# Optimization experiments

Measured on AMD Instinct MI355X. Metric: run time of the kernel, lower is better.

The kernel has to match this reference:

```python
import jax, jax.numpy as jnp
import numpy as np

H = W = 64      # patch grid (shape)
WS = 8          # window_size
SHIFT = 4       # shift_size (SW-MSA)
HEAD_DIM = 32
N = WS * WS     # tokens per window


def _rel_position_index(ws):
    coords = np.stack(np.meshgrid(np.arange(ws), np.arange(ws), indexing='ij'))  # (2, ws, ws)
    cf = coords.reshape(2, -1)
    rel = cf[:, :, None] - cf[:, None, :]            # (2, N, N)
    rel = rel.transpose(1, 2, 0).astype(np.int64)    # (N, N, 2)
    rel[..., 0] += ws - 1
    rel[..., 1] += ws - 1
    rel[..., 0] *= 2 * ws - 1
    return (rel[..., 0] + rel[..., 1]).astype(np.int32)  # (N, N), values in [0,(2ws-1)^2)


def _shift_mask(h, w, ws, shift):
    # Swin cyclic-shift attention mask: (num_windows, N, N) with 0 / -100
    img = np.zeros((h, w), dtype=np.float32)
    cnt = 0
    slices = (slice(0, -ws), slice(-ws, -shift), slice(-shift, None))
    for hs in slices:
        for ws_ in slices:
            img[hs, ws_] = cnt
            cnt += 1
    win = img.reshape(h // ws, ws, w // ws, ws).transpose(0, 2, 1, 3).reshape(-1, ws * ws)
    diff = win[:, None, :] - win[:, :, None]
    return np.where(diff != 0, np.float32(-100.0), np.float32(0.0))


def setup_inputs() -> dict:
    key = jax.random.key(0)
    ks = jax.random.split(key, 6)
    dim = 384
    B = 32
    sd = 1.0 / np.sqrt(dim)
    return {
        'x': jax.random.normal(ks[0], (B, H * W, dim), jnp.float32),
        'qkv_w': jax.random.normal(ks[1], (dim, 3 * dim), jnp.float32) * sd,
        'qkv_b': jnp.zeros((3 * dim,), jnp.float32),
        'proj_w': jax.random.normal(ks[2], (dim, dim), jnp.float32) * sd,
        'proj_b': jnp.zeros((dim,), jnp.float32),
        'bias_table': jax.random.normal(ks[3], ((2 * WS - 1) ** 2, dim // HEAD_DIM), jnp.float32) * 0.02,
        'rel_index': jnp.asarray(_rel_position_index(WS)),
    }


def reference(x, qkv_w, qkv_b, proj_w, proj_b, bias_table, rel_index):
    B, L, C = x.shape
    heads = C // HEAD_DIM
    scale = HEAD_DIM ** -0.5
    nh, nw = H // WS, W // WS

    xg = x.reshape(B, H, W, C)
    if SHIFT > 0:
        xg = jnp.roll(xg, shift=(-SHIFT, -SHIFT), axis=(1, 2))

    # window partition -> (B*nWin, N, C)
    xw = xg.reshape(B, nh, WS, nw, WS, C).transpose(0, 1, 3, 2, 4, 5).reshape(B * nh * nw, N, C)

    qkv = xw @ qkv_w + qkv_b                              # (Bw, N, 3C)
    q, k, v = jnp.split(qkv, 3, axis=-1)
    def heads_first(t):
        return t.reshape(-1, N, heads, HEAD_DIM).transpose(0, 2, 1, 3)  # (Bw, h, N, d)
    q, k, v = heads_first(q), heads_first(k), heads_first(v)

    attn = jnp.einsum('bhnd,bhmd->bhnm', q * scale, k)    # (Bw, h, N, N)
    bias = bias_table[rel_index]                          # (N, N, h)
    attn = attn + bias.transpose(2, 0, 1)[None]

    if SHIFT > 0:
        mask = jnp.asarray(_shift_mask(H, W, WS, SHIFT))  # (nWin, N, N), trace-time constant
        attn = attn.reshape(B, nh * nw, heads, N, N) + mask[None, :, None]
        attn = attn.reshape(B * nh * nw, heads, N, N)

    attn = jax.nn.softmax(attn, axis=-1)
    out = jnp.einsum('bhnm,bhmd->bhnd', attn, v)          # (Bw, h, N, d)
    out = out.transpose(0, 2, 1, 3).reshape(B * nh * nw, N, C)
    out = out @ proj_w + proj_b

    # window reverse
    out = out.reshape(B, nh, nw, WS, WS, C).transpose(0, 1, 3, 2, 4, 5).reshape(B, H, W, C)
    if SHIFT > 0:
        out = jnp.roll(out, shift=(SHIFT, SHIFT), axis=(1, 2))
    return out.reshape(B, L, C)
```

## Files before the change

### kernel.cpp

```cpp
#include <hip/hip_runtime.h>
#include <hip/hip_bf16.h>

#define CDIM 384
#define NQKV 1152
#define HEADS 12
#define SHIFT_ 4
#define SCALE_Q 0.17677669529663687f

typedef __attribute__((ext_vector_type(8))) short bf16x8;
typedef __attribute__((ext_vector_type(4))) float f32x4;
typedef __attribute__((ext_vector_type(4))) float float4_t;
typedef __attribute__((ext_vector_type(4))) unsigned u32x4;
typedef __attribute__((ext_vector_type(2))) unsigned u32x2;

__device__ inline short f2bf(float f) {
    union { float f; unsigned u; } v; v.f = f;
    unsigned r = v.u + 0x7FFFu + ((v.u >> 16) & 1u);
    return (short)(r >> 16);
}

__device__ inline unsigned cvtpk(float lo, float hi) {
    unsigned r;
    asm("v_cvt_pk_bf16_f32 %0, %1, %2" : "=v"(r) : "v"(lo), "v"(hi));
    return r;
}

__device__ inline bf16x8 mk8(unsigned w0, unsigned w1, unsigned w2, unsigned w3) {
    u32x4 t = {w0, w1, w2, w3};
    return __builtin_bit_cast(bf16x8, t);
}

__device__ inline bf16x8 pack8(float4_t a, float4_t b) {
    return mk8(cvtpk(a[0], a[1]), cvtpk(a[2], a[3]),
               cvtpk(b[0], b[1]), cvtpk(b[2], b[3]));
}

__device__ inline bf16x8 regroup(unsigned p0, unsigned p1, unsigned p2,
                                 unsigned p3, int lane) {
    int lhi = (lane >> 4) & 3;
    int s0 = (lane & 15) + ((lhi & 1) ? 32 : 0);
    int s1 = s0 + 16;
    unsigned a0 = __shfl(p0, s0), b0 = __shfl(p2, s0);
    unsigned a1 = __shfl(p1, s0), b1 = __shfl(p3, s0);
    unsigned a2 = __shfl(p0, s1), b2 = __shfl(p2, s1);
    unsigned a3 = __shfl(p1, s1), b3 = __shfl(p3, s1);
    bool hi = lhi >= 2;
    return mk8(hi ? b0 : a0, hi ? b1 : a1, hi ? b2 : a2, hi ? b3 : a3);
}

__device__ inline void gl16(const short* g, const short* l) {
    __builtin_amdgcn_global_load_lds((const __attribute__((address_space(1))) void*)g,
                                     (__attribute__((address_space(3))) void*)l, 16, 0, 0);
}

__device__ inline int invswz(int c) {
    int b2 = (c >> 2) & 1, b3 = (c >> 3) & 1, b4 = (c >> 4) & 1;
    return (c & ~7) | ((b2 ^ b4) << 2) | (((((c >> 1) & 1)) ^ b3) << 1) | ((c & 1) ^ b2 ^ b4);
}

__device__ inline int region_id(int wIdx, int tok) {
    int gh = ((wIdx >> 3) << 3) + (tok >> 3);
    int gw = (wIdx & 7) * 8 + (tok & 7);
    int rh = gh < 56 ? 0 : (gh < 60 ? 1 : 2);
    int rw = gw < 56 ? 0 : (gw < 60 ? 1 : 2);
    return rh * 3 + rw;
}

__device__ inline int crow(int row) { return row * 136 + (row >> 3) * 8; }

__device__ inline size_t xrow(int mg) {
    int tok = mg & 63, win = mg >> 6;
    int b = win >> 6, wIdx = win & 63;
    int gh = ((wIdx >> 3) << 3) + (tok >> 3);
    int gw = (wIdx & 7) * 8 + (tok & 7);
    int sh_ = (gh + SHIFT_) & 63, sw_ = (gw + SHIFT_) & 63;
    return (size_t)(b * 4096 + sh_ * 64 + sw_) * CDIM;
}

__global__ void prep_kernel(const float* __restrict__ qkv_w,
                            const float* __restrict__ proj_w,
                            const float* __restrict__ bias_table,
                            const int* __restrict__ rel_index,
                            short* __restrict__ qkvwt,
                            short* __restrict__ projwt,
                            float* __restrict__ biasP) {
    int t = blockIdx.x * 256 + threadIdx.x;
    if (t < NQKV * CDIM) {
        int n = t / CDIM, k = t - n * CDIM;
        qkvwt[t] = f2bf(qkv_w[k * NQKV + n]);
    }
    if (t < CDIM * CDIM) {
        int n = t / CDIM, k = t - n * CDIM;
        projwt[t] = f2bf(proj_w[k * CDIM + n]);
    }
    if (t < HEADS * 16 * 64 * 4) {
        int r = t & 3, lane = (t >> 2) & 63, g = (t >> 8) & 15, h = t >> 12;
        int kt = g >> 2, qt = g & 3;
        int key = kt * 16 + (lane >> 4) * 4 + r;
        int query = qt * 16 + (lane & 15);
        biasP[t] = bias_table[rel_index[query * 64 + key] * HEADS + h];
    }
}

__global__ __launch_bounds__(256) void gemm_qkv(
    const float* __restrict__ x, const short* __restrict__ wt,
    const float* __restrict__ qkv_b, short* __restrict__ qkbuf,
    short* __restrict__ vT)
{
    __shared__ alignas(16) char smemb[35072];
    short* As = (short*)smemb;
    short* Bs = As + 8192;
    short* Cst = (short*)smemb;
    int tid = threadIdx.x;
    int hw = blockIdx.x;
    int lb = (hw & 7) * 1152 + (hw >> 3);
    int bm = lb / 9, bn = lb - bm * 9;
    int m0 = bm * 128, n0 = bn * 128;

    int lane = tid & 63, wv = tid >> 6;
    int c0 = wv * 128 + lane, c1 = c0 + 64;
    const float* Asrc0 = x + xrow(m0 + (c0 >> 2)) + (c0 & 3) * 8;
    const float* Asrc1 = x + xrow(m0 + (c1 >> 2)) + (c1 & 3) * 8;
    short* Aw0 = As + (c0 ^ ((c0 >> 2) & 7)) * 8;
    short* Aw1 = As + (c1 ^ ((c1 >> 2) & 7)) * 8;
    int l0 = invswz(c0), l1 = invswz(c1);
    const short* Bg0 = wt + (size_t)(n0 + (l0 >> 2)) * CDIM + (l0 & 3) * 8;
    const short* Bg1 = wt + (size_t)(n0 + (l1 >> 2)) * CDIM + (l1 & 3) * 8;
    short* Bdst0 = Bs + wv * 1024;
    short* Bdst1 = Bdst0 + 512;

    int wr = wv >> 1, wc = wv & 1;
    int lrow = lane & 15, lhi = lane >> 4;
    int arow = wr * 64 + lrow, brow = wc * 64 + lrow;
    const short* ard = As + ((((arow * 64 + lhi * 16)) ^ ((lrow & 7) << 4)) >> 1);
    const short* brd = Bs + ((((brow * 64 + lhi * 16)) ^ ((lrow & 7) << 4)) >> 1);

    f32x4 zero = {0.f, 0.f, 0.f, 0.f};
    f32x4 acc[4][4];
    #pragma unroll
    for (int i = 0; i < 4; i++)
        #pragma unroll
        for (int j = 0; j < 4; j++) acc[i][j] = zero;

    float4_t sA0[4], sA1[4];
    {
        float4_t p0 = *(const float4_t*)(Asrc0);
        float4_t p1 = *(const float4_t*)(Asrc0 + 4);
        float4_t p2 = *(const float4_t*)(Asrc1);
        float4_t p3 = *(const float4_t*)(Asrc1 + 4);
        gl16(Bg0, Bdst0);
        gl16(Bg1, Bdst1);
        *(bf16x8*)Aw0 = pack8(p0, p1);
        *(bf16x8*)Aw1 = pack8(p2, p3);
        sA1[0] = *(const float4_t*)(Asrc0 + 32);
        sA1[1] = *(const float4_t*)(Asrc0 + 36);
        sA1[2] = *(const float4_t*)(Asrc1 + 32);
        sA1[3] = *(const float4_t*)(Asrc1 + 36);
    }
    __syncthreads();

    #pragma unroll
    for (int ks = 0; ks < 12; ks++) {
        int cur = (ks & 1) * 4096, nxt = 4096 - cur;
        if (ks < 11) {
            if ((ks + 1) & 1) {
                *(bf16x8*)(Aw0 + nxt) = pack8(sA1[0], sA1[1]);
                *(bf16x8*)(Aw1 + nxt) = pack8(sA1[2], sA1[3]);
            } else {
                *(bf16x8*)(Aw0 + nxt) = pack8(sA0[0], sA0[1]);
                *(bf16x8*)(Aw1 + nxt) = pack8(sA0[2], sA0[3]);
            }
            int k1 = (ks + 1) * 32;
            gl16(Bg0 + k1, Bdst0 + nxt);
            gl16(Bg1 + k1, Bdst1 + nxt);
        }
        if (ks < 10) {
            int k2 = (ks + 2) * 32;
            if (ks & 1) {
                sA1[0] = *(const float4_t*)(Asrc0 + k2);
                sA1[1] = *(const float4_t*)(Asrc0 + k2 + 4);
                sA1[2] = *(const float4_t*)(Asrc1 + k2);
                sA1[3] = *(const float4_t*)(Asrc1 + k2 + 4);
            } else {
                sA0[0] = *(const float4_t*)(Asrc0 + k2);
                sA0[1] = *(const float4_t*)(Asrc0 + k2 + 4);
                sA0[2] = *(const float4_t*)(Asrc1 + k2);
                sA0[3] = *(const float4_t*)(Asrc1 + k2 + 4);
            }
        }
        bf16x8 af[4], bfr[4];
        #pragma unroll
        for (int t = 0; t < 4; t++) af[t]  = *(const bf16x8*)(ard + cur + t * 512);
        #pragma unroll
        for (int t = 0; t < 4; t++) bfr[t] = *(const bf16x8*)(brd + cur + t * 512);
        __builtin_amdgcn_s_setprio(1);
        #pragma unroll
        for (int i = 0; i < 4; i++)
            #pragma unroll
            for (int j = 0; j < 4; j++)
                acc[i][j] = __builtin_amdgcn_mfma_f32_16x16x32_bf16(af[i], bfr[j], acc[i][j], 0, 0, 0);
        __builtin_amdgcn_s_setprio(0);
        __syncthreads();
    }
    #pragma unroll
    for (int tj = 0; tj < 4; tj++) {
        int col = wc * 64 + tj * 16 + lrow;
        int cg = n0 + col;
        float bias = qkv_b[cg];
        float sc = (cg < CDIM) ? SCALE_Q : 1.0f;
        #pragma unroll
        for (int ti = 0; ti < 4; ti++) {
            int row0 = wr * 64 + ti * 16 + lhi * 4;
            #pragma unroll
            for (int r = 0; r < 4; r++)
                Cst[crow(row0 + r) + col] = f2bf((acc[ti][tj][r] + bias) * sc);
        }
    }
    __syncthreads();
    if (bn < 6) {
        #pragma unroll
        for (int i = 0; i < 8; i++) {
            int rr = i * 16 + (tid >> 4);
            int cc = (tid & 15) * 8;
            bf16x8 v = *(const bf16x8*)(Cst + crow(rr) + cc);
            __builtin_nontemporal_store(v,
                (bf16x8*)(qkbuf + (size_t)(m0 + rr) * 768 + n0 + cc));
        }
    } else {
        #pragma unroll
        for (int it = 0; it < 8; it++) {
            int t = it * 256 + tid;
            int col = t >> 4, tk8 = t & 15;
            bf16x8 v;
            #pragma unroll
            for (int j = 0; j < 8; j++)
                v[j] = Cst[crow(tk8 * 8 + j) + col];
            int win = bm * 2 + (tk8 >> 3);
            int head = (bn - 6) * 4 + (col >> 5);
            int dim = col & 31;
            __builtin_nontemporal_store(v,
                (bf16x8*)(vT + (((size_t)win * HEADS + head) * 32 + dim) * 64 + (tk8 & 7) * 8));
        }
    }
}

__global__ __launch_bounds__(256) void attn_reg(
    const short* __restrict__ qkbuf, const short* __restrict__ vT,
    const float* __restrict__ biasP, short* __restrict__ attno)
{
    int tid = threadIdx.x;
    int lane = tid & 63, wv = tid >> 6;
    int lrow = lane & 15, lhi = lane >> 4;
    int w = blockIdx.x;
    int wIdx = w & 63;
    bool needmask = ((wIdx >> 3) == 7) || ((wIdx & 7) == 7);

    int rq[4], rk[4][4];
    #pragma unroll
    for (int qt = 0; qt < 4; qt++) rq[qt] = region_id(wIdx, qt * 16 + lrow);
    #pragma unroll
    for (int kt = 0; kt < 4; kt++)
        #pragma unroll
        for (int r = 0; r < 4; r++)
            rk[kt][r] = region_id(wIdx, kt * 16 + lhi * 4 + r);

    f32x4 zero = {0.f, 0.f, 0.f, 0.f};
    const short* qbase = qkbuf + (size_t)(w * 64) * 768;

    for (int hi = 0; hi < 3; hi++) {
        int h = wv * 3 + hi;
        bf16x8 kf[4];
        #pragma unroll
        for (int kt = 0; kt < 4; kt++)
            kf[kt] = __builtin_nontemporal_load(
                (const bf16x8*)(qbase + (size_t)(kt * 16 + lrow) * 768 + CDIM + h * 32 + lhi * 8));
        bf16x8 pa[4][2];
        #pragma unroll
        for (int qt = 0; qt < 4; qt++) {
            bf16x8 qf = __builtin_nontemporal_load(
                (const bf16x8*)(qbase + (size_t)(qt * 16 + lrow) * 768 + h * 32 + lhi * 8));
            f32x4 st[4];
            __builtin_amdgcn_s_setprio(1);
            #pragma unroll
            for (int kt = 0; kt < 4; kt++)
                st[kt] = __builtin_amdgcn_mfma_f32_16x16x32_bf16(kf[kt], qf, zero, 0, 0, 0);
            __builtin_amdgcn_s_setprio(0);
            float pv[16]; float sum = 0.f;
            #pragma unroll
            for (int kt = 0; kt < 4; kt++) {
                f32x4 bb = *(const f32x4*)(biasP + (((size_t)h * 16 + kt * 4 + qt) * 64 + lane) * 4);
                #pragma unroll
                for (int r = 0; r < 4; r++) {
                    float p = __expf(st[kt][r] + bb[r]);
                    p = (needmask && (rq[qt] != rk[kt][r])) ? 0.f : p;
                    pv[kt * 4 + r] = p; sum += p;
                }
            }
            sum += __shfl_xor(sum, 16);
            sum += __shfl_xor(sum, 32);
            float rcp = 1.0f / sum;
            unsigned a0 = cvtpk(pv[0] * rcp, pv[1] * rcp);
            unsigned a1 = cvtpk(pv[2] * rcp, pv[3] * rcp);
            unsigned a2 = cvtpk(pv[4] * rcp, pv[5] * rcp);
            unsigned a3 = cvtpk(pv[6] * rcp, pv[7] * rcp);
            pa[qt][0] = regroup(a0, a1, a2, a3, lane);
            a0 = cvtpk(pv[8] * rcp,  pv[9] * rcp);
            a1 = cvtpk(pv[10] * rcp, pv[11] * rcp);
            a2 = cvtpk(pv[12] * rcp, pv[13] * rcp);
            a3 = cvtpk(pv[14] * rcp, pv[15] * rcp);
            pa[qt][1] = regroup(a0, a1, a2, a3, lane);
        }
        const short* vb = vT + ((size_t)w * HEADS + h) * 32 * 64;
        bf16x8 vfrag[2][2];
        #pragma unroll
        for (int ks2 = 0; ks2 < 2; ks2++)
            #pragma unroll
            for (int dt = 0; dt < 2; dt++)
                vfrag[ks2][dt] = __builtin_nontemporal_load(
                    (const bf16x8*)(vb + (size_t)(dt * 16 + lrow) * 64 + ks2 * 32 + lhi * 8));
        f32x4 ao2[4][2];
        #pragma unroll
        for (int qt = 0; qt < 4; qt++) { ao2[qt][0] = zero; ao2[qt][1] = zero; }
        __builtin_amdgcn_s_setprio(1);
        #pragma unroll
        for (int ks2 = 0; ks2 < 2; ks2++)
            #pragma unroll
            for (int qt = 0; qt < 4; qt++) {
                ao2[qt][0] = __builtin_amdgcn_mfma_f32_16x16x32_bf16(vfrag[ks2][0], pa[qt][ks2], ao2[qt][0], 0, 0, 0);
                ao2[qt][1] = __builtin_amdgcn_mfma_f32_16x16x32_bf16(vfrag[ks2][1], pa[qt][ks2], ao2[qt][1], 0, 0, 0);
            }
        __builtin_amdgcn_s_setprio(0);
        short* abase = attno + (size_t)(w * 64) * CDIM + h * 32 + lhi * 4;
        #pragma unroll
        for (int qt = 0; qt < 4; qt++) {
            int token = qt * 16 + lrow;
            short* p0 = abase + (size_t)token * CDIM;
            u32x2 s0, s1;
            s0[0] = cvtpk(ao2[qt][0][0], ao2[qt][0][1]);
            s0[1] = cvtpk(ao2[qt][0][2], ao2[qt][0][3]);
            s1[0] = cvtpk(ao2[qt][1][0], ao2[qt][1][1]);
            s1[1] = cvtpk(ao2[qt][1][2], ao2[qt][1][3]);
            __builtin_nontemporal_store(s0, (u32x2*)(p0));
            __builtin_nontemporal_store(s1, (u32x2*)(p0 + 16));
        }
    }
}

__global__ __launch_bounds__(256) void gemm_proj(
    const short* __restrict__ a, const short* __restrict__ wt,
    const float* __restrict__ proj_b, float* __restrict__ out)
{
    __shared__ alignas(16) short As[8192];
    __shared__ alignas(16) short Bs[8192];
    int tid = threadIdx.x;
    int hw = blockIdx.x;
    int lb = (hw & 7) * 384 + (hw >> 3);
    int bm = lb / 3, bn = lb - bm * 3;
    int m0 = bm * 128, n0 = bn * 128;

    int lane = tid & 63, wv = tid >> 6;
    int c0 = wv * 128 + lane, c1 = c0 + 64;
    int l0 = invswz(c0), l1 = invswz(c1);
    const short* Ag0 = a + (size_t)(m0 + (l0 >> 2)) * CDIM + (l0 & 3) * 8;
    const short* Ag1 = a + (size_t)(m0 + (l1 >> 2)) * CDIM + (l1 & 3) * 8;
    const short* Bg0 = wt + (size_t)(n0 + (l0 >> 2)) * CDIM + (l0 & 3) * 8;
    const short* Bg1 = wt + (size_t)(n0 + (l1 >> 2)) * CDIM + (l1 & 3) * 8;
    short* Adst0 = As + wv * 1024;
    short* Adst1 = Adst0 + 512;
    short* Bdst0 = Bs + wv * 1024;
    short* Bdst1 = Bdst0 + 512;

    int wr = wv >> 1, wc = wv & 1;
    int lrow = lane & 15, lhi = lane >> 4;
    int arow = wr * 64 + lrow, brow = wc * 64 + lrow;
    const short* ard = As + ((((arow * 64 + lhi * 16)) ^ ((lrow & 7) << 4)) >> 1);
    const short* brd = Bs + ((((brow * 64 + lhi * 16)) ^ ((lrow & 7) << 4)) >> 1);

    f32x4 zero = {0.f, 0.f, 0.f, 0.f};
    f32x4 acc[4][4];
    #pragma unroll
    for (int i = 0; i < 4; i++)
        #pragma unroll
        for (int j = 0; j < 4; j++) acc[i][j] = zero;

    gl16(Ag0, Adst0);
    gl16(Bg0, Bdst0);
    gl16(Ag1, Adst1);
    gl16(Bg1, Bdst1);
    __syncthreads();

    #pragma unroll
    for (int ks = 0; ks < 12; ks++) {
        int cur = (ks & 1) * 4096, nxt = 4096 - cur;
        if (ks < 11) {
            int k1 = (ks + 1) * 32;
            gl16(Ag0 + k1, Adst0 + nxt);
            gl16(Bg0 + k1, Bdst0 + nxt);
            gl16(Ag1 + k1, Adst1 + nxt);
            gl16(Bg1 + k1, Bdst1 + nxt);
        }
        bf16x8 af[4], bfr[4];
        #pragma unroll
        for (int t = 0; t < 4; t++) af[t]  = *(const bf16x8*)(ard + cur + t * 512);
        #pragma unroll
        for (int t = 0; t < 4; t++) bfr[t] = *(const bf16x8*)(brd + cur + t * 512);
        __builtin_amdgcn_s_setprio(1);
        #pragma unroll
        for (int i = 0; i < 4; i++)
            #pragma unroll
            for (int j = 0; j < 4; j++)
                acc[i][j] = __builtin_amdgcn_mfma_f32_16x16x32_bf16(af[i], bfr[j], acc[i][j], 0, 0, 0);
        __builtin_amdgcn_s_setprio(0);
        __syncthreads();
    }
    #pragma unroll
    for (int ti = 0; ti < 4; ti++) {
        #pragma unroll
        for (int r = 0; r < 4; r++) {
            int m = m0 + wr * 64 + ti * 16 + lhi * 4 + r;
            int b = m >> 12, wIdx = (m >> 6) & 63, tok = m & 63;
            int gh = ((wIdx >> 3) << 3) + (tok >> 3);
            int gw = (wIdx & 7) * 8 + (tok & 7);
            int ih = (gh + SHIFT_) & 63, iw = (gw + SHIFT_) & 63;
            size_t ob = ((size_t)(b << 12) + ih * 64 + iw) * CDIM;
            #pragma unroll
            for (int tj = 0; tj < 4; tj++) {
                int col = n0 + wc * 64 + tj * 16 + lrow;
                float v = acc[ti][tj][r] + proj_b[col];
                __builtin_nontemporal_store(v, &out[ob + col]);
            }
        }
    }
}

extern "C" void kernel_launch(void* const* d_in, const int* in_sizes, int n_in,
                              void* d_out, int out_size, void* d_ws, size_t ws_size,
                              hipStream_t stream) {
    const float* x          = (const float*)d_in[0];
    const float* qkv_w      = (const float*)d_in[1];
    const float* qkv_b      = (const float*)d_in[2];
    const float* proj_w     = (const float*)d_in[3];
    const float* proj_b     = (const float*)d_in[4];
    const float* bias_table = (const float*)d_in[5];
    const int*   rel_index  = (const int*)d_in[6];
    float* out = (float*)d_out;
    char* ws = (char*)d_ws;

    short* qkvwt = (short*)(ws);
    short* projwt = (short*)(ws + 884736);
    float* biasP  = (float*)(ws + 1179648);
    short* qkbuf  = (short*)(ws + 1376256);
    short* vT     = (short*)(ws + 202702848);
    short* attno  = (short*)(ws + 303366144);

    prep_kernel<<<1728, 256, 0, stream>>>(qkv_w, proj_w, bias_table, rel_index,
                                          qkvwt, projwt, biasP);
    gemm_qkv<<<9216, 256, 0, stream>>>(x, qkvwt, qkv_b, qkbuf, vT);
    attn_reg<<<2048, 256, 0, stream>>>(qkbuf, vT, biasP, attno);
    gemm_proj<<<3072, 256, 0, stream>>>(attno, projwt, proj_b, out);
}
```

Baseline: 432.1 us.

## Triple-buffer QKV GEMM weight tiles with two-stage prefetch and partial waitcnt

The B (weight) tiles in the QKV GEMM get a three-slot LDS ring and are prefetched two k-steps ahead via direct global-to-LDS loads, while A stays double-buffered. The full __syncthreads is replaced by an explicit s_waitcnt vmcnt(6) plus s_barrier, so the newest global loads can stay in flight across the barrier. The aim is to hide weight-load latency behind the MFMA work. It costs more LDS per block, which may lower occupancy. It also depends on exact vmcnt accounting in the last iterations, where no new loads are issued.

```diff
diff --git a/kernel.cpp b/kernel.cpp
--- a/kernel.cpp
+++ b/kernel.cpp
@@ -107,7 +107,7 @@
     const float* __restrict__ qkv_b, short* __restrict__ qkbuf,
     short* __restrict__ vT)
 {
-    __shared__ alignas(16) char smemb[35072];
+    __shared__ alignas(16) char smemb[40960];
     short* As = (short*)smemb;
     short* Bs = As + 8192;
     short* Cst = (short*)smemb;
@@ -144,35 +144,44 @@
 
     float4_t sA0[4], sA1[4];
     {
-        float4_t p0 = *(const float4_t*)(Asrc0);
-        float4_t p1 = *(const float4_t*)(Asrc0 + 4);
-        float4_t p2 = *(const float4_t*)(Asrc1);
-        float4_t p3 = *(const float4_t*)(Asrc1 + 4);
+        sA0[0] = *(const float4_t*)(Asrc0);
+        sA0[1] = *(const float4_t*)(Asrc0 + 4);
+        sA0[2] = *(const float4_t*)(Asrc1);
+        sA0[3] = *(const float4_t*)(Asrc1 + 4);
         gl16(Bg0, Bdst0);
         gl16(Bg1, Bdst1);
-        *(bf16x8*)Aw0 = pack8(p0, p1);
-        *(bf16x8*)Aw1 = pack8(p2, p3);
+        gl16(Bg0 + 32, Bdst0 + 4096);
+        gl16(Bg1 + 32, Bdst1 + 4096);
+        *(bf16x8*)Aw0 = pack8(sA0[0], sA0[1]);
+        *(bf16x8*)Aw1 = pack8(sA0[2], sA0[3]);
         sA1[0] = *(const float4_t*)(Asrc0 + 32);
         sA1[1] = *(const float4_t*)(Asrc0 + 36);
         sA1[2] = *(const float4_t*)(Asrc1 + 32);
         sA1[3] = *(const float4_t*)(Asrc1 + 36);
     }
-    __syncthreads();
+    __builtin_amdgcn_sched_barrier(0);
+    asm volatile("s_waitcnt vmcnt(6) lgkmcnt(0)");
+    __builtin_amdgcn_s_barrier();
+    __builtin_amdgcn_sched_barrier(0);
 
     #pragma unroll
     for (int ks = 0; ks < 12; ks++) {
-        int cur = (ks & 1) * 4096, nxt = 4096 - cur;
+        int curA = (ks & 1) * 4096, nxtA = 4096 - curA;
+        int curB = (ks % 3) * 4096;
+        if (ks < 10) {
+            int k2 = (ks + 2) * 32;
+            int b2 = ((ks + 2) % 3) * 4096;
+            gl16(Bg0 + k2, Bdst0 + b2);
+            gl16(Bg1 + k2, Bdst1 + b2);
+        }
         if (ks < 11) {
             if ((ks + 1) & 1) {
-                *(bf16x8*)(Aw0 + nxt) = pack8(sA1[0], sA1[1]);
-                *(bf16x8*)(Aw1 + nxt) = pack8(sA1[2], sA1[3]);
+                *(bf16x8*)(Aw0 + nxtA) = pack8(sA1[0], sA1[1]);
+                *(bf16x8*)(Aw1 + nxtA) = pack8(sA1[2], sA1[3]);
             } else {
-                *(bf16x8*)(Aw0 + nxt) = pack8(sA0[0], sA0[1]);
-                *(bf16x8*)(Aw1 + nxt) = pack8(sA0[2], sA0[3]);
+                *(bf16x8*)(Aw0 + nxtA) = pack8(sA0[0], sA0[1]);
+                *(bf16x8*)(Aw1 + nxtA) = pack8(sA0[2], sA0[3]);
             }
-            int k1 = (ks + 1) * 32;
-            gl16(Bg0 + k1, Bdst0 + nxt);
-            gl16(Bg1 + k1, Bdst1 + nxt);
         }
         if (ks < 10) {
             int k2 = (ks + 2) * 32;
@@ -190,9 +199,9 @@
         }
         bf16x8 af[4], bfr[4];
         #pragma unroll
-        for (int t = 0; t < 4; t++) af[t]  = *(const bf16x8*)(ard + cur + t * 512);
-        #pragma unroll
-        for (int t = 0; t < 4; t++) bfr[t] = *(const bf16x8*)(brd + cur + t * 512);
+        for (int t = 0; t < 4; t++) af[t]  = *(const bf16x8*)(ard + curA + t * 512);
+        #pragma unroll
+        for (int t = 0; t < 4; t++) bfr[t] = *(const bf16x8*)(brd + curB + t * 512);
         __builtin_amdgcn_s_setprio(1);
         #pragma unroll
         for (int i = 0; i < 4; i++)
@@ -200,7 +209,10 @@
             for (int j = 0; j < 4; j++)
                 acc[i][j] = __builtin_amdgcn_mfma_f32_16x16x32_bf16(af[i], bfr[j], acc[i][j], 0, 0, 0);
         __builtin_amdgcn_s_setprio(0);
-        __syncthreads();
+        __builtin_amdgcn_sched_barrier(0);
+        asm volatile("s_waitcnt vmcnt(6) lgkmcnt(0)");
+        __builtin_amdgcn_s_barrier();
+        __builtin_amdgcn_sched_barrier(0);
     }
     #pragma unroll
     for (int tj = 0; tj < 4; tj++) {
```

Result: no change. 439.1 us (+1.6%).
